# Kernel optimization log

Measured on AMD Instinct MI355X. Metric: run time of the kernel, lower is better.

The kernel has to match this reference:

```python
import jax, jax.numpy as jnp
import numpy as np

SEQ, BATCH, D_MODEL = 2048, 2, 1024
NHEAD = 16
HEAD_DIM = D_MODEL // NHEAD
D_FF = 4096
LN_EPS = 1e-5
ROPE_THETA = 10000.0


def _rope_cos_sin(seq_len, dim, dtype):
    # lucidrains RotaryEmbedding: inv_freq over even indices, interleaved repeat
    inv_freq = 1.0 / (ROPE_THETA ** (jnp.arange(0, dim, 2, dtype=jnp.float32) / dim))
    t = jnp.arange(seq_len, dtype=jnp.float32)
    freqs = t[:, None] * inv_freq[None, :]            # [S, dim/2]
    freqs = jnp.repeat(freqs, 2, axis=-1)             # [S, dim] (f0,f0,f1,f1,...)
    return jnp.cos(freqs).astype(dtype), jnp.sin(freqs).astype(dtype)


def _rotate_half(x):
    # interleaved pairs: (x0,x1,x2,x3,...) -> (-x1,x0,-x3,x2,...)
    x = x.reshape(x.shape[:-1] + (-1, 2))
    x1, x2 = x[..., 0], x[..., 1]
    return jnp.stack([-x2, x1], axis=-1).reshape(x.shape[:-2] + (-1,))


def _apply_rope(x, cos, sin):
    # x: [B, H, S, D]; cos/sin: [S, D]
    return x * cos[None, None, :, :] + _rotate_half(x) * sin[None, None, :, :]


def _layer_norm(x, g, b):
    mu = jnp.mean(x, axis=-1, keepdims=True)
    var = jnp.mean(jnp.square(x - mu), axis=-1, keepdims=True)
    return (x - mu) * jax.lax.rsqrt(var + LN_EPS) * g + b


def setup_inputs() -> dict:
    key = jax.random.key(0)
    ks = jax.random.split(key, 12)
    s = 1.0 / np.sqrt(D_MODEL)
    sf = 1.0 / np.sqrt(D_FF)
    return {
        "src": jax.random.normal(ks[0], (SEQ, BATCH, D_MODEL), jnp.float32),
        "q_w": jax.random.uniform(ks[1], (D_MODEL, D_MODEL), jnp.float32, -s, s),
        "q_b": jnp.zeros((D_MODEL,), jnp.float32),
        "k_w": jax.random.uniform(ks[2], (D_MODEL, D_MODEL), jnp.float32, -s, s),
        "k_b": jnp.zeros((D_MODEL,), jnp.float32),
        "v_w": jax.random.uniform(ks[3], (D_MODEL, D_MODEL), jnp.float32, -s, s),
        "v_b": jnp.zeros((D_MODEL,), jnp.float32),
        "w1": jax.random.uniform(ks[4], (D_MODEL, D_FF), jnp.float32, -s, s),
        "b1": jnp.zeros((D_FF,), jnp.float32),
        "w2": jax.random.uniform(ks[5], (D_FF, D_MODEL), jnp.float32, -sf, sf),
        "b2": jnp.zeros((D_MODEL,), jnp.float32),
        "ln1_g": jnp.ones((D_MODEL,), jnp.float32),
        "ln1_b": jnp.zeros((D_MODEL,), jnp.float32),
        "ln2_g": jnp.ones((D_MODEL,), jnp.float32),
        "ln2_b": jnp.zeros((D_MODEL,), jnp.float32),
    }


def reference(src, q_w, q_b, k_w, k_b, v_w, v_b, w1, b1, w2, b2,
              ln1_g, ln1_b, ln2_g, ln2_b):
    S, B, E = src.shape
    q = src @ q_w + q_b
    k = src @ k_w + k_b
    v = src @ v_w + v_b
    # [S,B,E] -> [B,H,S,D]
    def split_heads(x):
        return x.reshape(S, B, NHEAD, HEAD_DIM).transpose(1, 2, 0, 3)
    q, k, v = split_heads(q), split_heads(k), split_heads(v)
    cos, sin = _rope_cos_sin(S, HEAD_DIM, src.dtype)
    q = _apply_rope(q, cos, sin)
    k = _apply_rope(k, cos, sin)
    scores = jnp.einsum("bhqd,bhkd->bhqk", q, k) / np.sqrt(HEAD_DIM)
    probs = jax.nn.softmax(scores, axis=-1)
    out = jnp.einsum("bhqk,bhkd->bhqd", probs, v)      # [B,H,S,D]
    out = out.transpose(2, 0, 1, 3).reshape(S, B, E)
    x = _layer_norm(src + out, ln1_g, ln1_b)
    ff = (jax.nn.relu(x @ w1 + b1)) @ w2 + b2
    return _layer_norm(x + ff, ln2_g, ln2_b)
```

## Files before the change

### kernel.cpp

```cpp
#include <hip/hip_runtime.h>
#include <hip/hip_bf16.h>

#define SEQ 2048
#define BATCH 2
#define DMODEL 1024
#define NHEAD 16
#define HDIM 64
#define DFF 4096
#define LN_EPS 1e-5f
#define QKVSZ (BATCH * NHEAD * SEQ * HDIM)

typedef unsigned short ushort_t;
typedef __attribute__((ext_vector_type(8))) short short8;
typedef __attribute__((ext_vector_type(4))) float floatx4;

__device__ __forceinline__ float bf2f(ushort_t u) {
    union { unsigned int i; float f; } v;
    v.i = ((unsigned int)u) << 16;
    return v.f;
}
__device__ __forceinline__ ushort_t f2bf(float f) {
    union { float f; unsigned int i; } v;
    v.f = f;
    unsigned int r = v.i + 0x7fffu + ((v.i >> 16) & 1u);
    return (ushort_t)(r >> 16);
}
__device__ __forceinline__ void gload_lds16(const ushort_t* g, ushort_t* l) {
    __builtin_amdgcn_global_load_lds(
        (const __attribute__((address_space(1))) void*)g,
        (__attribute__((address_space(3))) void*)l, 16, 0, 0);
}

__global__ __launch_bounds__(256) void sniff_kernel(const ushort_t* __restrict__ qw,
                                                    int* __restrict__ flag) {
    float mx = 0.f;
    for (int i = threadIdx.x; i < 4096; i += 256) {
        float v = fabsf(bf2f(qw[i]));
        if (v <= 3.0e38f) mx = fmaxf(mx, v);
    }
#pragma unroll
    for (int off = 1; off < 64; off <<= 1) mx = fmaxf(mx, __shfl_xor(mx, off, 64));
    __shared__ float sm[4];
    if ((threadIdx.x & 63) == 0) sm[threadIdx.x >> 6] = mx;
    __syncthreads();
    if (threadIdx.x == 0) {
        float m = fmaxf(fmaxf(sm[0], sm[1]), fmaxf(sm[2], sm[3]));
        *flag = (m > 1.0f) ? 1 : 0;
    }
}

__global__ __launch_bounds__(256) void convert_kernel(const void* __restrict__ src,
                                                      ushort_t* __restrict__ dst,
                                                      int n, const int* __restrict__ flag) {
    const int f = *flag;
    int i = blockIdx.x * 256 + threadIdx.x;
    const int stride = gridDim.x * 256;
    if (f) {
        const float* s = (const float*)src;
        for (; i < n; i += stride) dst[i] = f2bf(s[i]);
    } else {
        const ushort_t* s = (const ushort_t*)src;
        for (; i < n; i += stride) dst[i] = s[i];
    }
}

__global__ __launch_bounds__(256) void transpose_convert_kernel(
    const void* __restrict__ src, ushort_t* __restrict__ dst,
    int K, int N, const int* __restrict__ flag)
{
    __shared__ ushort_t tile[64][72];
    const int n0 = blockIdx.x * 64, k0 = blockIdx.y * 64;
    const int tx = threadIdx.x & 63, ty = threadIdx.x >> 6;
    const int f = *flag;
    if (f) {
        const float* s = (const float*)src;
#pragma unroll
        for (int i = 0; i < 16; i++) {
            int r = ty + 4 * i;
            tile[r][tx] = f2bf(s[(size_t)(k0 + r) * N + n0 + tx]);
        }
    } else {
        const ushort_t* s = (const ushort_t*)src;
#pragma unroll
        for (int i = 0; i < 16; i++) {
            int r = ty + 4 * i;
            tile[r][tx] = s[(size_t)(k0 + r) * N + n0 + tx];
        }
    }
    __syncthreads();
#pragma unroll
    for (int i = 0; i < 16; i++) {
        int r = ty + 4 * i;
        dst[(size_t)(n0 + r) * K + k0 + tx] = tile[tx][r];
    }
}

__global__ __launch_bounds__(256) void rope_table_kernel(float* __restrict__ tab) {
    int idx = blockIdx.x * 256 + threadIdx.x;
    int s = idx >> 5, i = idx & 31;
    float inv = exp2f(-(float)(2 * i) * (13.287712379549449f / 64.f));
    float ang = (float)s * inv;
    tab[idx * 2 + 0] = cosf(ang);
    tab[idx * 2 + 1] = sinf(ang);
}

template <int MODE>
__global__ __launch_bounds__(256) void gemm_kernel(
    const ushort_t* __restrict__ A, const ushort_t* __restrict__ BT,
    const ushort_t* __restrict__ bias, void* __restrict__ out,
    void* __restrict__ out2, const float* __restrict__ rope,
    int M, int N, int K)
{
    __shared__ ushort_t sA[128 * 32];
    __shared__ ushort_t sB[128 * 32];

    const int tid = threadIdx.x;
    const int lane = tid & 63;
    const int w = tid >> 6;
    const int wm = (w >> 1) * 64;
    const int wn = (w & 1) * 64;
    const int m0 = blockIdx.y * 128;
    const int n0 = blockIdx.x * 128;

    const int Kc = (MODE == 3) ? (K >> 1) : K;
    const int kbeg = (MODE == 3) ? (int)blockIdx.z * Kc : 0;

    floatx4 acc[4][4];
#pragma unroll
    for (int i = 0; i < 4; i++)
#pragma unroll
        for (int j = 0; j < 4; j++) {
            floatx4 z = {0.f, 0.f, 0.f, 0.f};
            acc[i][j] = z;
        }

    const int srow = tid >> 2;
    const int scol = (tid & 3) * 8;
    const ushort_t* Ag = A + (size_t)(m0 + srow) * K + scol + kbeg;
    const ushort_t* Bg = BT + (size_t)(n0 + srow) * K + scol + kbeg;
    ushort_t* ldsA0 = sA + w * 512;
    ushort_t* ldsA1 = sA + 2048 + w * 512;
    ushort_t* ldsB0 = sB + w * 512;
    ushort_t* ldsB1 = sB + 2048 + w * 512;
    const size_t rstep = (size_t)64 * K;

    for (int k0 = 0; k0 < Kc; k0 += 32) {
        gload_lds16(Ag + k0, ldsA0);
        gload_lds16(Ag + rstep + k0, ldsA1);
        gload_lds16(Bg + k0, ldsB0);
        gload_lds16(Bg + rstep + k0, ldsB1);
        __syncthreads();

        short8 a[4], b[4];
#pragma unroll
        for (int mt = 0; mt < 4; mt++)
            a[mt] = *(const short8*)&sA[(wm + mt * 16 + (lane & 15)) * 32 + (lane >> 4) * 8];
#pragma unroll
        for (int nt = 0; nt < 4; nt++)
            b[nt] = *(const short8*)&sB[(wn + nt * 16 + (lane & 15)) * 32 + (lane >> 4) * 8];
#pragma unroll
        for (int mt = 0; mt < 4; mt++)
#pragma unroll
            for (int nt = 0; nt < 4; nt++)
                acc[mt][nt] = __builtin_amdgcn_mfma_f32_16x16x32_bf16(
                    a[mt], b[nt], acc[mt][nt], 0, 0, 0);
        __syncthreads();
    }

#pragma unroll
    for (int mt = 0; mt < 4; mt++) {
#pragma unroll
        for (int nt = 0; nt < 4; nt++) {
#pragma unroll
            for (int r = 0; r < 4; r++) {
                int row = wm + mt * 16 + (lane >> 4) * 4 + r;
                int col = wn + nt * 16 + (lane & 15);
                int m = m0 + row, n = n0 + col;
                float val = acc[mt][nt][r];
                if (MODE != 3) val += bf2f(bias[n]);
                if (MODE == 1) {
                    int mat = n >> 10, nn = n & 1023;
                    int h = nn >> 6, d = nn & 63;
                    int s = m >> 1, bb = m & 1;
                    if (mat < 2) {
                        int i = d >> 1;
                        float c  = rope[((size_t)s * 32 + i) * 2 + 0];
                        float sn = rope[((size_t)s * 32 + i) * 2 + 1];
                        float partner = __shfl_xor(val, 1, 64);
                        val = (d & 1) ? (val * c + partner * sn)
                                      : (val * c - partner * sn);
                        if (mat == 0) val *= 0.18033688011112042f;
                    }
                    size_t off;
                    if (mat == 2)
                        off = (size_t)2 * QKVSZ + ((size_t)(bb * NHEAD + h) * HDIM + d) * SEQ + s;
                    else
                        off = (size_t)mat * QKVSZ + ((size_t)(bb * NHEAD + h) * SEQ + s) * HDIM + d;
                    ((ushort_t*)out)[off] = f2bf(val);
                } else if (MODE == 2) {
                    ((ushort_t*)out)[(size_t)m * N + n] = f2bf(fmaxf(val, 0.f));
                } else {
                    float* outp = blockIdx.z ? (float*)out2 : (float*)out;
                    outp[(size_t)m * N + n] = val;
                }
            }
        }
    }
}

__global__ __launch_bounds__(256) void attn_kernel(
    const ushort_t* __restrict__ Q, const ushort_t* __restrict__ K,
    const ushort_t* __restrict__ VT, ushort_t* __restrict__ out)
{
    __shared__ ushort_t sQ[128][72];
    __shared__ ushort_t sK[64][72];
    __shared__ ushort_t sVT[64][72];
    __shared__ ushort_t sP[128][72];

    const int tid = threadIdx.x;
    const int lane = tid & 63;
    const int w = tid >> 6;
    const int quad = lane >> 4;
    const int l15 = lane & 15;
    const int bh = blockIdx.y;
    const int q0 = blockIdx.x * 128;

    const ushort_t* Qg  = Q + ((size_t)bh * SEQ + q0) * HDIM;
    const ushort_t* Kg  = K + (size_t)bh * SEQ * HDIM;
    const ushort_t* VTg = VT + (size_t)bh * SEQ * HDIM;

#pragma unroll
    for (int p = 0; p < 4; p++) {
        int chunk = tid + p * 256;
        int r = chunk >> 3, c = (chunk & 7) * 8;
        *(short8*)&sQ[r][c] = *(const short8*)(Qg + (size_t)r * HDIM + c);
    }
    __syncthreads();
    short8 aQ[2][2];
#pragma unroll
    for (int mt = 0; mt < 2; mt++)
#pragma unroll
        for (int kk = 0; kk < 2; kk++)
            aQ[mt][kk] = *(const short8*)&sQ[w * 32 + mt * 16 + l15][kk * 32 + quad * 8];

    floatx4 accO[2][4];
    floatx4 accL[2];
#pragma unroll
    for (int mt = 0; mt < 2; mt++) {
        floatx4 z = {0.f, 0.f, 0.f, 0.f};
        accL[mt] = z;
#pragma unroll
        for (int nt = 0; nt < 4; nt++) accO[mt][nt] = z;
    }
    short8 ones;
#pragma unroll
    for (int j = 0; j < 8; j++) ones[j] = (short)0x3F80;

    for (int kv0 = 0; kv0 < SEQ; kv0 += 64) {
        __syncthreads();
#pragma unroll
        for (int p = 0; p < 2; p++) {
            int chunk = tid + p * 256;
            int r = chunk >> 3, c = (chunk & 7) * 8;
            *(short8*)&sK[r][c]  = *(const short8*)(Kg + (size_t)(kv0 + r) * HDIM + c);
            *(short8*)&sVT[r][c] = *(const short8*)(VTg + (size_t)r * SEQ + kv0 + c);
        }
        __syncthreads();

        floatx4 accS[2][4];
#pragma unroll
        for (int mt = 0; mt < 2; mt++)
#pragma unroll
            for (int nt = 0; nt < 4; nt++) {
                floatx4 z = {0.f, 0.f, 0.f, 0.f};
                accS[mt][nt] = z;
            }
#pragma unroll
        for (int kk = 0; kk < 2; kk++)
#pragma unroll
            for (int nt = 0; nt < 4; nt++) {
                short8 bK = *(const short8*)&sK[nt * 16 + l15][kk * 32 + quad * 8];
#pragma unroll
                for (int mt = 0; mt < 2; mt++)
                    accS[mt][nt] = __builtin_amdgcn_mfma_f32_16x16x32_bf16(
                        aQ[mt][kk], bK, accS[mt][nt], 0, 0, 0);
            }

#pragma unroll
        for (int mt = 0; mt < 2; mt++)
#pragma unroll
            for (int nt = 0; nt < 4; nt++)
#pragma unroll
                for (int r = 0; r < 4; r++)
                    sP[w * 32 + mt * 16 + quad * 4 + r][nt * 16 + l15] =
                        f2bf(exp2f(accS[mt][nt][r]));

#pragma unroll
        for (int mt = 0; mt < 2; mt++) {
#pragma unroll
            for (int kkp = 0; kkp < 2; kkp++) {
                short8 aP = *(const short8*)&sP[w * 32 + mt * 16 + l15][kkp * 32 + quad * 8];
#pragma unroll
                for (int nt = 0; nt < 4; nt++) {
                    short8 bV = *(const short8*)&sVT[nt * 16 + l15][kkp * 32 + quad * 8];
                    accO[mt][nt] = __builtin_amdgcn_mfma_f32_16x16x32_bf16(
                        aP, bV, accO[mt][nt], 0, 0, 0);
                }
                accL[mt] = __builtin_amdgcn_mfma_f32_16x16x32_bf16(
                    aP, ones, accL[mt], 0, 0, 0);
            }
        }
    }

    const int b = bh >> 4, h = bh & 15;
#pragma unroll
    for (int mt = 0; mt < 2; mt++) {
        float rinv[4];
#pragma unroll
        for (int r = 0; r < 4; r++) rinv[r] = 1.0f / accL[mt][r];
#pragma unroll
        for (int nt = 0; nt < 4; nt++)
#pragma unroll
            for (int r = 0; r < 4; r++) {
                int qrow = q0 + w * 32 + mt * 16 + quad * 4 + r;
                int d = nt * 16 + l15;
                out[((size_t)qrow * BATCH + b) * DMODEL + h * HDIM + d] =
                    f2bf(accO[mt][nt][r] * rinv[r]);
            }
    }
}

__global__ __launch_bounds__(256) void ln1_kernel(
    const ushort_t* __restrict__ src, ushort_t* io,
    const ushort_t* __restrict__ g, const ushort_t* __restrict__ bb)
{
    const int row = blockIdx.x;
    const int tid = threadIdx.x;
    const size_t base = (size_t)row * DMODEL;
    const int j0 = tid * 4;
    float v[4];
#pragma unroll
    for (int j = 0; j < 4; j++)
        v[j] = bf2f(src[base + j0 + j]) + bf2f(io[base + j0 + j]);

    float s = v[0] + v[1] + v[2] + v[3];
    float ss = v[0] * v[0] + v[1] * v[1] + v[2] * v[2] + v[3] * v[3];
#pragma unroll
    for (int off = 1; off < 64; off <<= 1) {
        s += __shfl_xor(s, off, 64);
        ss += __shfl_xor(ss, off, 64);
    }
    __shared__ float ps[4], pss[4];
    if ((tid & 63) == 0) { ps[tid >> 6] = s; pss[tid >> 6] = ss; }
    __syncthreads();
    s = ps[0] + ps[1] + ps[2] + ps[3];
    ss = pss[0] + pss[1] + pss[2] + pss[3];
    float mu = s * (1.f / DMODEL);
    float var = ss * (1.f / DMODEL) - mu * mu;
    float rstd = rsqrtf(var + LN_EPS);
#pragma unroll
    for (int j = 0; j < 4; j++) {
        float y = (v[j] - mu) * rstd * bf2f(g[j0 + j]) + bf2f(bb[j0 + j]);
        io[base + j0 + j] = f2bf(y);
    }
}

__global__ __launch_bounds__(256) void ln2_kernel(
    const ushort_t* __restrict__ xb, float* io,
    const float* __restrict__ ff1, const ushort_t* __restrict__ b2,
    const ushort_t* __restrict__ g, const ushort_t* __restrict__ bb)
{
    const int row = blockIdx.x;
    const int tid = threadIdx.x;
    const size_t base = (size_t)row * DMODEL;
    const int j0 = tid * 4;
    float v[4];
#pragma unroll
    for (int j = 0; j < 4; j++)
        v[j] = bf2f(xb[base + j0 + j]) + io[base + j0 + j] + ff1[base + j0 + j]
             + bf2f(b2[j0 + j]);

    float s = v[0] + v[1] + v[2] + v[3];
    float ss = v[0] * v[0] + v[1] * v[1] + v[2] * v[2] + v[3] * v[3];
#pragma unroll
    for (int off = 1; off < 64; off <<= 1) {
        s += __shfl_xor(s, off, 64);
        ss += __shfl_xor(ss, off, 64);
    }
    __shared__ float ps[4], pss[4];
    if ((tid & 63) == 0) { ps[tid >> 6] = s; pss[tid >> 6] = ss; }
    __syncthreads();
    s = ps[0] + ps[1] + ps[2] + ps[3];
    ss = pss[0] + pss[1] + pss[2] + pss[3];
    float mu = s * (1.f / DMODEL);
    float var = ss * (1.f / DMODEL) - mu * mu;
    float rstd = rsqrtf(var + LN_EPS);
#pragma unroll
    for (int j = 0; j < 4; j++) {
        float y = (v[j] - mu) * rstd * bf2f(g[j0 + j]) + bf2f(bb[j0 + j]);
        io[base + j0 + j] = y;
    }
}

extern "C" void kernel_launch(void* const* d_in, const int* in_sizes, int n_in,
                              void* d_out, int out_size, void* d_ws, size_t ws_size,
                              hipStream_t stream)
{
    char* ws = (char*)d_ws;
    const size_t MB = 1024 * 1024;
    const size_t KB = 1024;

    ushort_t* c_src   = (ushort_t*)(ws + 0);
    ushort_t* c_wqkvT = (ushort_t*)(ws + 8 * MB);
    ushort_t* c_w1T   = (ushort_t*)(ws + 14 * MB);
    ushort_t* c_w2T   = (ushort_t*)(ws + 22 * MB);
    char* sp = ws + 30 * MB;
    ushort_t* c_qkvb  = (ushort_t*)(sp + 0 * KB);
    ushort_t* c_b1    = (ushort_t*)(sp + 8 * KB);
    ushort_t* c_b2    = (ushort_t*)(sp + 16 * KB);
    ushort_t* c_ln1g  = (ushort_t*)(sp + 20 * KB);
    ushort_t* c_ln1b  = (ushort_t*)(sp + 24 * KB);
    ushort_t* c_ln2g  = (ushort_t*)(sp + 28 * KB);
    ushort_t* c_ln2b  = (ushort_t*)(sp + 32 * KB);
    int*      flag    = (int*)(sp + 36 * KB);
    float*    rope    = (float*)(ws + 30 * MB + 512 * KB);
    ushort_t* QKVb    = (ushort_t*)(ws + 31 * MB);
    ushort_t* attn_xb = (ushort_t*)(ws + 63 * MB);
    ushort_t* hbuf    = (ushort_t*)(ws + 31 * MB);
    float*    ffb1    = (float*)(ws + 0);
    float*    ffb0    = (float*)d_out;

    const int M = SEQ * BATCH;
    dim3 blk(256);

    sniff_kernel<<<dim3(1), blk, 0, stream>>>((const ushort_t*)d_in[1], flag);

    transpose_convert_kernel<<<dim3(16, 16), blk, 0, stream>>>(d_in[1], c_wqkvT + 0 * DMODEL * DMODEL, DMODEL, DMODEL, flag);
    transpose_convert_kernel<<<dim3(16, 16), blk, 0, stream>>>(d_in[3], c_wqkvT + 1 * DMODEL * DMODEL, DMODEL, DMODEL, flag);
    transpose_convert_kernel<<<dim3(16, 16), blk, 0, stream>>>(d_in[5], c_wqkvT + 2 * DMODEL * DMODEL, DMODEL, DMODEL, flag);
    transpose_convert_kernel<<<dim3(64, 16), blk, 0, stream>>>(d_in[7], c_w1T, DMODEL, DFF, flag);
    transpose_convert_kernel<<<dim3(16, 64), blk, 0, stream>>>(d_in[9], c_w2T, DFF, DMODEL, flag);

    auto conv = [&](int idx, ushort_t* dst, int n) {
        int grid = (n + 255) / 256;
        if (grid > 2048) grid = 2048;
        convert_kernel<<<dim3(grid), blk, 0, stream>>>(d_in[idx], dst, n, flag);
    };
    conv(0,  c_src,  SEQ * BATCH * DMODEL);
    conv(2,  c_qkvb + 0 * DMODEL, DMODEL);
    conv(4,  c_qkvb + 1 * DMODEL, DMODEL);
    conv(6,  c_qkvb + 2 * DMODEL, DMODEL);
    conv(8,  c_b1,   DFF);
    conv(10, c_b2,   DMODEL);
    conv(11, c_ln1g, DMODEL);
    conv(12, c_ln1b, DMODEL);
    conv(13, c_ln2g, DMODEL);
    conv(14, c_ln2b, DMODEL);

    rope_table_kernel<<<dim3(SEQ * 32 / 256), blk, 0, stream>>>(rope);

    gemm_kernel<1><<<dim3(3 * DMODEL / 128, M / 128), blk, 0, stream>>>(
        c_src, c_wqkvT, c_qkvb, QKVb, nullptr, rope, M, 3 * DMODEL, DMODEL);

    attn_kernel<<<dim3(SEQ / 128, BATCH * NHEAD), blk, 0, stream>>>(
        QKVb, QKVb + QKVSZ, QKVb + 2 * QKVSZ, attn_xb);

    ln1_kernel<<<dim3(M), blk, 0, stream>>>(c_src, attn_xb, c_ln1g, c_ln1b);

    gemm_kernel<2><<<dim3(DFF / 128, M / 128), blk, 0, stream>>>(
        attn_xb, c_w1T, c_b1, hbuf, nullptr, rope, M, DFF, DMODEL);

    gemm_kernel<3><<<dim3(DMODEL / 128, M / 128, 2), blk, 0, stream>>>(
        hbuf, c_w2T, c_b2, ffb0, ffb1, rope, M, DMODEL, DFF);

    ln2_kernel<<<dim3(M), blk, 0, stream>>>(attn_xb, ffb0, ffb1, c_b2, c_ln2g, c_ln2b);
}
```

Measured before the change: 423.8 us.

## Double attention KV tile to 128, reuse Q smem for P, swizzle P writes

Processes 128 keys per outer iteration in two 64-key halves, which halves the number of barrier-separated global-to-shared loads. The Q shared buffer is reused to hold P once Q has been read into registers, so total LDS stays roughly similar. P stores get an XOR swizzle to reduce bank conflicts, V fragments are hoisted and shared across both mt tiles, and the bf16 rounding is simplified to round-half-up. The risks are a larger LDS footprint, more register pressure, and a slight numeric difference from the cheaper rounding.

```diff
diff --git a/kernel.cpp b/kernel.cpp
--- a/kernel.cpp
+++ b/kernel.cpp
@@ -212,18 +212,17 @@
     const ushort_t* __restrict__ Q, const ushort_t* __restrict__ K,
     const ushort_t* __restrict__ VT, ushort_t* __restrict__ out)
 {
-    __shared__ ushort_t sQ[128][72];
-    __shared__ ushort_t sK[64][72];
-    __shared__ ushort_t sVT[64][72];
-    __shared__ ushort_t sP[128][72];
-
-    const int tid = threadIdx.x;
+    __shared__ ushort_t sQP[128 * 72];
+    __shared__ ushort_t sK[128 * 72];
+    __shared__ ushort_t sVT[64 * 136];
+
+    const int tid  = threadIdx.x;
     const int lane = tid & 63;
-    const int w = tid >> 6;
+    const int w    = tid >> 6;
     const int quad = lane >> 4;
-    const int l15 = lane & 15;
-    const int bh = blockIdx.y;
-    const int q0 = blockIdx.x * 128;
+    const int l15  = lane & 15;
+    const int bh   = blockIdx.y;
+    const int q0   = blockIdx.x * 128;
 
     const ushort_t* Qg  = Q + ((size_t)bh * SEQ + q0) * HDIM;
     const ushort_t* Kg  = K + (size_t)bh * SEQ * HDIM;
@@ -233,7 +232,7 @@
     for (int p = 0; p < 4; p++) {
         int chunk = tid + p * 256;
         int r = chunk >> 3, c = (chunk & 7) * 8;
-        *(short8*)&sQ[r][c] = *(const short8*)(Qg + (size_t)r * HDIM + c);
+        *(short8*)&sQP[r * 72 + c] = *(const short8*)(Qg + (size_t)r * HDIM + c);
     }
     __syncthreads();
     short8 aQ[2][2];
@@ -241,7 +240,7 @@
     for (int mt = 0; mt < 2; mt++)
 #pragma unroll
         for (int kk = 0; kk < 2; kk++)
-            aQ[mt][kk] = *(const short8*)&sQ[w * 32 + mt * 16 + l15][kk * 32 + quad * 8];
+            aQ[mt][kk] = *(const short8*)&sQP[(w * 32 + mt * 16 + l15) * 72 + kk * 32 + quad * 8];
 
     floatx4 accO[2][4];
     floatx4 accL[2];
@@ -256,58 +255,74 @@
 #pragma unroll
     for (int j = 0; j < 8; j++) ones[j] = (short)0x3F80;
 
-    for (int kv0 = 0; kv0 < SEQ; kv0 += 64) {
+    for (int kv0 = 0; kv0 < SEQ; kv0 += 128) {
         __syncthreads();
 #pragma unroll
-        for (int p = 0; p < 2; p++) {
+        for (int p = 0; p < 4; p++) {
             int chunk = tid + p * 256;
-            int r = chunk >> 3, c = (chunk & 7) * 8;
-            *(short8*)&sK[r][c]  = *(const short8*)(Kg + (size_t)(kv0 + r) * HDIM + c);
-            *(short8*)&sVT[r][c] = *(const short8*)(VTg + (size_t)r * SEQ + kv0 + c);
+            int rk = chunk >> 3, ck = (chunk & 7) * 8;
+            *(short8*)&sK[rk * 72 + ck] =
+                *(const short8*)(Kg + (size_t)(kv0 + rk) * HDIM + ck);
+            int rv = chunk >> 4, cv = (chunk & 15) * 8;
+            *(short8*)&sVT[rv * 136 + cv] =
+                *(const short8*)(VTg + (size_t)rv * SEQ + kv0 + cv);
         }
         __syncthreads();
 
-        floatx4 accS[2][4];
-#pragma unroll
-        for (int mt = 0; mt < 2; mt++)
-#pragma unroll
-            for (int nt = 0; nt < 4; nt++) {
-                floatx4 z = {0.f, 0.f, 0.f, 0.f};
-                accS[mt][nt] = z;
-            }
-#pragma unroll
-        for (int kk = 0; kk < 2; kk++)
-#pragma unroll
-            for (int nt = 0; nt < 4; nt++) {
-                short8 bK = *(const short8*)&sK[nt * 16 + l15][kk * 32 + quad * 8];
-#pragma unroll
-                for (int mt = 0; mt < 2; mt++)
-                    accS[mt][nt] = __builtin_amdgcn_mfma_f32_16x16x32_bf16(
-                        aQ[mt][kk], bK, accS[mt][nt], 0, 0, 0);
-            }
-
-#pragma unroll
-        for (int mt = 0; mt < 2; mt++)
-#pragma unroll
-            for (int nt = 0; nt < 4; nt++)
-#pragma unroll
-                for (int r = 0; r < 4; r++)
-                    sP[w * 32 + mt * 16 + quad * 4 + r][nt * 16 + l15] =
-                        f2bf(exp2f(accS[mt][nt][r]));
-
-#pragma unroll
-        for (int mt = 0; mt < 2; mt++) {
+#pragma unroll
+        for (int half = 0; half < 2; half++) {
+            floatx4 accS[2][4];
+#pragma unroll
+            for (int mt = 0; mt < 2; mt++)
+#pragma unroll
+                for (int nt = 0; nt < 4; nt++) {
+                    floatx4 z = {0.f, 0.f, 0.f, 0.f};
+                    accS[mt][nt] = z;
+                }
+#pragma unroll
+            for (int kk = 0; kk < 2; kk++)
+#pragma unroll
+                for (int nt = 0; nt < 4; nt++) {
+                    short8 bK = *(const short8*)
+                        &sK[(half * 64 + nt * 16 + l15) * 72 + kk * 32 + quad * 8];
+#pragma unroll
+                    for (int mt = 0; mt < 2; mt++)
+                        accS[mt][nt] = __builtin_amdgcn_mfma_f32_16x16x32_bf16(
+                            aQ[mt][kk], bK, accS[mt][nt], 0, 0, 0);
+                }
+
+#pragma unroll
+            for (int mt = 0; mt < 2; mt++)
+#pragma unroll
+                for (int nt = 0; nt < 4; nt++)
+#pragma unroll
+                    for (int r = 0; r < 4; r++) {
+                        int row = w * 32 + mt * 16 + quad * 4 + r;
+                        union { float f; unsigned int i; } u;
+                        u.f = exp2f(accS[mt][nt][r]);
+                        int idx = (row * 72 + nt * 16 + l15) ^ (((row >> 2) & 3) << 3);
+                        sQP[idx] = (ushort_t)((u.i + 0x8000u) >> 16);
+                    }
+
 #pragma unroll
             for (int kkp = 0; kkp < 2; kkp++) {
-                short8 aP = *(const short8*)&sP[w * 32 + mt * 16 + l15][kkp * 32 + quad * 8];
-#pragma unroll
-                for (int nt = 0; nt < 4; nt++) {
-                    short8 bV = *(const short8*)&sVT[nt * 16 + l15][kkp * 32 + quad * 8];
-                    accO[mt][nt] = __builtin_amdgcn_mfma_f32_16x16x32_bf16(
-                        aP, bV, accO[mt][nt], 0, 0, 0);
+                short8 bV[4];
+#pragma unroll
+                for (int nt = 0; nt < 4; nt++)
+                    bV[nt] = *(const short8*)
+                        &sVT[(nt * 16 + l15) * 136 + half * 64 + kkp * 32 + quad * 8];
+#pragma unroll
+                for (int mt = 0; mt < 2; mt++) {
+                    int prow = w * 32 + mt * 16 + l15;
+                    int pidx = (prow * 72 + kkp * 32 + quad * 8) ^ (((prow >> 2) & 3) << 3);
+                    short8 aP = *(const short8*)&sQP[pidx];
+#pragma unroll
+                    for (int nt = 0; nt < 4; nt++)
+                        accO[mt][nt] = __builtin_amdgcn_mfma_f32_16x16x32_bf16(
+                            aP, bV[nt], accO[mt][nt], 0, 0, 0);
+                    accL[mt] = __builtin_amdgcn_mfma_f32_16x16x32_bf16(
+                        aP, ones, accL[mt], 0, 0, 0);
                 }
-                accL[mt] = __builtin_amdgcn_mfma_f32_16x16x32_bf16(
-                    aP, ones, accL[mt], 0, 0, 0);
             }
         }
     }
```

New measurement: 436.1 us. 2.9% more time.
